# Kernel optimization log

Measured on AMD Instinct MI355X. Metric: run time of the kernel, lower is better.

Reference implementation:

```python
import jax, jax.numpy as jnp
import numpy as np

B, S, H = 2, 2048, 2048
N = 16               # num heads
NOPE, ROPE, V = 128, 64, 128
QHD = NOPE + ROPE    # 192 per-head q/k dim
QL, KVL = 1536, 512  # q_lora_rank, kv_lora_rank
THETA = 10000.0
SCALE = QHD ** -0.5
EPS = 1e-6


def rmsnorm(x, w):
    var = jnp.mean(x.astype(jnp.float32) ** 2, axis=-1, keepdims=True)
    return (x.astype(jnp.float32) * jax.lax.rsqrt(var + EPS)).astype(x.dtype) * w


def rotate_half(x):
    d = x.shape[-1] // 2
    return jnp.concatenate([-x[..., d:], x[..., :d]], axis=-1)


def setup_inputs() -> dict:
    key = jax.random.key(0)
    ks = jax.random.split(key, 8)
    w = lambda k, shape: jax.random.normal(k, shape, jnp.float32) * 0.02
    return {
        "hidden_states": jax.random.normal(ks[0], (B, S, H), jnp.float32),
        "position_ids": (jnp.arange(B * S, dtype=jnp.int64) % 4096).reshape(B, S),
        "q_a_w": w(ks[1], (QL, H)),
        "q_a_ln_w": jnp.ones((QL,), jnp.float32),
        "q_b_w": w(ks[2], (N * QHD, QL)),
        "kv_a_w": w(ks[3], (KVL + ROPE, H)),
        "kv_a_ln_w": jnp.ones((KVL,), jnp.float32),
        "kv_b_w": w(ks[4], (N * (NOPE + V), KVL)),
        "o_w": w(ks[5], (H, N * V)),
    }


def mla_forward(hidden_states, position_ids, q_a_w, q_a_ln_w, q_b_w,
                kv_a_w, kv_a_ln_w, kv_b_w, o_w):
    b, s, _ = hidden_states.shape
    # ---- Q low-rank path: q_b(rmsnorm(q_a(x))) ----
    q = rmsnorm(hidden_states @ q_a_w.T, q_a_ln_w) @ q_b_w.T
    q = q.reshape(b, s, N, QHD)
    q_nope, q_pe = q[..., :NOPE], q[..., NOPE:]
    # ---- compressed KV + shared rope key ----
    kv_a = hidden_states @ kv_a_w.T                       # [b,s,KVL+ROPE]
    compressed_kv = rmsnorm(kv_a[..., :KVL], kv_a_ln_w)   # [b,s,KVL]
    k_pe = kv_a[..., KVL:].reshape(b, s, 1, ROPE)         # MQA rope key
    # ---- RoPE (default, theta=1e4) from position_ids ----
    inv_freq = 1.0 / (THETA ** (jnp.arange(0, ROPE, 2, dtype=jnp.float32) / ROPE))
    freqs = position_ids.astype(jnp.float32)[..., None] * inv_freq  # [b,s,ROPE/2]
    emb = jnp.concatenate([freqs, freqs], axis=-1)                  # [b,s,ROPE]
    cos = jnp.cos(emb)[:, :, None, :].astype(hidden_states.dtype)   # [b,s,1,ROPE]
    sin = jnp.sin(emb)[:, :, None, :].astype(hidden_states.dtype)
    q_pe = q_pe * cos + rotate_half(q_pe) * sin
    k_pe = k_pe * cos + rotate_half(k_pe) * sin
    # ---- decompress latent KV via kv_b_proj ----
    kv = (compressed_kv @ kv_b_w.T).reshape(b, s, N, NOPE + V)
    k_nope, v = kv[..., :NOPE], kv[..., NOPE:]
    k = jnp.concatenate([k_nope, jnp.broadcast_to(k_pe, (b, s, N, ROPE))], axis=-1)
    qf = jnp.concatenate([q_nope, q_pe], axis=-1)          # [b,s,N,QHD]
    # ---- causal SDPA in bsnd layout ----
    scores = jnp.einsum('bqnd,bknd->bnqk', qf, k) * SCALE  # [b,N,s,s]
    causal = jnp.tril(jnp.ones((s, s), bool))
    scores = jnp.where(causal, scores, jnp.finfo(scores.dtype).min)
    probs = jax.nn.softmax(scores, axis=-1)
    attn = jnp.einsum('bnqk,bknd->bqnd', probs, v)         # [b,s,N,V]
    out = attn.reshape(b, s, N * V) @ o_w.T
    return out


def reference(hidden_states, position_ids, q_a_w, q_a_ln_w, q_b_w,
              kv_a_w, kv_a_ln_w, kv_b_w, o_w):
    return mla_forward(hidden_states, position_ids, q_a_w, q_a_ln_w, q_b_w,
                       kv_a_w, kv_a_ln_w, kv_b_w, o_w)
```

## Files before the change

kernel.cpp:

```cpp
#include <hip/hip_runtime.h>
#include <cstdio>

typedef unsigned short u16;
typedef u16 u16x8 __attribute__((ext_vector_type(8)));
typedef __bf16 bf16x8 __attribute__((ext_vector_type(8)));
typedef float f32x4 __attribute__((ext_vector_type(4)));

#define AS1 __attribute__((address_space(1)))
#define AS3 __attribute__((address_space(3)))

#define GLOAD16(gsrc, ldst) __builtin_amdgcn_global_load_lds( \
    (const AS1 void*)(gsrc), (AS3 void*)(ldst), 16, 0, 0)

__device__ __forceinline__ u16 f2bf(float f) {
  unsigned u = __builtin_bit_cast(unsigned, f);
  u += 0x7fffu + ((u >> 16) & 1u);
  return (u16)(u >> 16);
}
__device__ __forceinline__ float bf2f(u16 h) {
  return __builtin_bit_cast(float, (unsigned)h << 16);
}

__global__ __launch_bounds__(256) void cvt_pad_k(const float* __restrict__ src,
                                                 u16* __restrict__ dst,
                                                 long srcN, long dstN) {
  long i = ((long)blockIdx.x * 256 + threadIdx.x) * 8;
  const long stride = (long)gridDim.x * 256 * 8;
  for (; i < dstN; i += stride) {
    u16x8 o = {0,0,0,0,0,0,0,0};
    if (i < srcN) {
      const float4* p = (const float4*)(src + i);
      float4 a = p[0], b = p[1];
      o[0]=f2bf(a.x); o[1]=f2bf(a.y); o[2]=f2bf(a.z); o[3]=f2bf(a.w);
      o[4]=f2bf(b.x); o[5]=f2bf(b.y); o[6]=f2bf(b.z); o[7]=f2bf(b.w);
    }
    *(u16x8*)(dst + i) = o;
  }
}

__global__ __launch_bounds__(256) void rms_k(const u16* __restrict__ src, u16* __restrict__ dst,
                                             const float* __restrict__ w,
                                             int sstride, int dstride, int cols) {
  const int row = blockIdx.x;
  const int tid = threadIdx.x;
  const int nch = cols >> 3;
  float x[8];
  float ss = 0.f;
  if (tid < nch) {
    u16x8 v = *(const u16x8*)(src + (size_t)row * sstride + tid * 8);
#pragma unroll
    for (int j = 0; j < 8; ++j) { x[j] = bf2f(v[j]); ss += x[j] * x[j]; }
  } else {
#pragma unroll
    for (int j = 0; j < 8; ++j) x[j] = 0.f;
  }
#pragma unroll
  for (int off = 1; off < 64; off <<= 1) ss += __shfl_xor(ss, off);
  __shared__ float red[4];
  const int wv = tid >> 6, ln = tid & 63;
  if (ln == 0) red[wv] = ss;
  __syncthreads();
  const float tot = red[0] + red[1] + red[2] + red[3];
  const float rs = 1.0f / sqrtf(tot / (float)cols + 1e-6f);
  if (tid < nch) {
    u16x8 o;
#pragma unroll
    for (int j = 0; j < 8; ++j) o[j] = f2bf(x[j] * rs * w[tid * 8 + j]);
    *(u16x8*)(dst + (size_t)row * dstride + tid * 8) = o;
  }
}

__global__ __launch_bounds__(256) void rope_k(u16* __restrict__ q, const u16* __restrict__ kva,
                                              u16* __restrict__ kpe, const int* __restrict__ pos) {
  const int tok = blockIdx.x;
  const int j = threadIdx.x & 63;
  const int w = threadIdx.x >> 6;
  const float p = (float)pos[tok];
  const int jj = j & 31;
  const float inv = __powf(10000.0f, -(float)jj * (1.0f / 32.0f));
  float s, c;
  __sincosf(p * inv, &s, &c);
  const float sgn = (j < 32) ? -1.0f : 1.0f;
  const int partner = (j < 32) ? j + 32 : j - 32;
  if (w == 0) {
    const float x  = bf2f(kva[(size_t)tok * 640 + 512 + j]);
    const float xp = bf2f(kva[(size_t)tok * 640 + 512 + partner]);
    kpe[(size_t)tok * 64 + j] = f2bf(x * c + sgn * xp * s);
  }
#pragma unroll
  for (int hh = 0; hh < 4; ++hh) {
    const int h = w * 4 + hh;
    const size_t base = (size_t)tok * 3072 + h * 192 + 128;
    const float x  = bf2f(q[base + j]);
    const float xp = bf2f(q[base + partner]);
    q[base + j] = f2bf(x * c + sgn * xp * s);
  }
}

__global__ __launch_bounds__(256) void gemm_bt(const u16* __restrict__ A, const u16* __restrict__ B,
                                               u16* __restrict__ Cb, float* __restrict__ Cf,
                                               int M, int N, int K) {
  __shared__ __attribute__((aligned(16))) u16 As[128 * 64];
  __shared__ __attribute__((aligned(16))) u16 Bs[128 * 64];
  const int tid = threadIdx.x;
  const int m0 = blockIdx.y * 128, n0 = blockIdx.x * 128;
  const int w = tid >> 6, lane = tid & 63;
  const int wr = w >> 1, wc = w & 1;
  const int lr = lane & 15, g = lane >> 4;

  f32x4 acc[4][4] = {};

  for (int k0 = 0; k0 < K; k0 += 64) {
#pragma unroll
    for (int i = 0; i < 4; ++i) {
      const int c = i * 256 + tid;
      const int row = c >> 3, col = (c & 7) << 3;
      GLOAD16(A + (size_t)(m0 + row) * K + k0 + col, &As[c * 8]);
    }
#pragma unroll
    for (int i = 0; i < 4; ++i) {
      const int c = i * 256 + tid;
      const int row = c >> 3, col = (c & 7) << 3;
      GLOAD16(B + (size_t)(n0 + row) * K + k0 + col, &Bs[c * 8]);
    }
    __syncthreads();
    bf16x8 af[4][2], bfr[4][2];
#pragma unroll
    for (int x = 0; x < 4; ++x)
#pragma unroll
      for (int kk = 0; kk < 2; ++kk) {
        af[x][kk]  = *(const bf16x8*)(&As[(wr * 64 + x * 16 + lr) * 64 + kk * 32 + g * 8]);
        bfr[x][kk] = *(const bf16x8*)(&Bs[(wc * 64 + x * 16 + lr) * 64 + kk * 32 + g * 8]);
      }
#pragma unroll
    for (int mi = 0; mi < 4; ++mi)
#pragma unroll
      for (int ni = 0; ni < 4; ++ni)
#pragma unroll
        for (int kk = 0; kk < 2; ++kk)
          acc[mi][ni] = __builtin_amdgcn_mfma_f32_16x16x32_bf16(af[mi][kk], bfr[ni][kk],
                                                                acc[mi][ni], 0, 0, 0);
    __syncthreads();
  }

  const int rb = m0 + wr * 64, cb = n0 + wc * 64;
#pragma unroll
  for (int mi = 0; mi < 4; ++mi)
#pragma unroll
    for (int ni = 0; ni < 4; ++ni)
#pragma unroll
      for (int i = 0; i < 4; ++i) {
        const int r = rb + mi * 16 + g * 4 + i;
        const int cI = cb + ni * 16 + lr;
        if (Cf) Cf[(size_t)r * N + cI] = acc[mi][ni][i];
        else    Cb[(size_t)r * N + cI] = f2bf(acc[mi][ni][i]);
      }
}

__global__ __launch_bounds__(512) void gemm256(const u16* __restrict__ A, const u16* __restrict__ B,
                                               u16* __restrict__ Cb, float* __restrict__ Cf,
                                               int M, int N, int K) {
  __shared__ __attribute__((aligned(16))) u16 As[2][256 * 64];
  __shared__ __attribute__((aligned(16))) u16 Bs[2][256 * 64];
  const int tid = threadIdx.x;
  const int m0 = blockIdx.y * 256, n0 = blockIdx.x * 256;
  const int wid = tid >> 6, lane = tid & 63;
  const int wr = wid >> 2, wc = wid & 3;
  const int lr = lane & 15, g = lane >> 4;

  const u16* pA[4];
  const u16* pB[4];
  int lOff[4];
#pragma unroll
  for (int i = 0; i < 4; ++i) {
    const int c = i * 512 + tid;
    const int row = c >> 3, cl = c & 7;
    const int cg = cl ^ (row & 7);
    lOff[i] = c * 8;
    pA[i] = A + (size_t)(m0 + row) * K + cg * 8;
    pB[i] = B + (size_t)(n0 + row) * K + cg * 8;
  }

  const int aBase = (wr * 128 + lr) * 64;
  const int bBase = (wc * 64 + lr) * 64;
  int kch[2];
#pragma unroll
  for (int kk = 0; kk < 2; ++kk) kch[kk] = ((kk * 4 + g) ^ (lr & 7)) * 8;

  f32x4 acc[8][4] = {};
  const int nkt = K >> 6;

#pragma unroll
  for (int i = 0; i < 4; ++i) GLOAD16(pA[i], &As[0][lOff[i]]);
#pragma unroll
  for (int i = 0; i < 4; ++i) GLOAD16(pB[i], &Bs[0][lOff[i]]);
#pragma unroll
  for (int i = 0; i < 4; ++i) { pA[i] += 64; pB[i] += 64; }
  asm volatile("s_waitcnt vmcnt(0)" ::: "memory");
  __builtin_amdgcn_s_barrier();
  __builtin_amdgcn_sched_barrier(0);

  for (int t = 0; t < nkt; ++t) {
    const int buf = t & 1;
    if (t + 1 < nkt) {
#pragma unroll
      for (int i = 0; i < 4; ++i) GLOAD16(pA[i], &As[buf ^ 1][lOff[i]]);
#pragma unroll
      for (int i = 0; i < 4; ++i) GLOAD16(pB[i], &Bs[buf ^ 1][lOff[i]]);
#pragma unroll
      for (int i = 0; i < 4; ++i) { pA[i] += 64; pB[i] += 64; }
    }
    bf16x8 bfr[4][2];
#pragma unroll
    for (int fn = 0; fn < 4; ++fn)
#pragma unroll
      for (int kk = 0; kk < 2; ++kk)
        bfr[fn][kk] = *(const bf16x8*)(&Bs[buf][bBase + fn * 1024 + kch[kk]]);
#pragma unroll
    for (int q = 0; q < 4; ++q) {
      bf16x8 afr[2][2];
#pragma unroll
      for (int fr = 0; fr < 2; ++fr)
#pragma unroll
        for (int kk = 0; kk < 2; ++kk)
          afr[fr][kk] = *(const bf16x8*)(&As[buf][aBase + (q * 2 + fr) * 1024 + kch[kk]]);
      asm volatile("s_waitcnt lgkmcnt(0)" ::: "memory");
      __builtin_amdgcn_sched_barrier(0);
      __builtin_amdgcn_s_setprio(1);
#pragma unroll
      for (int fr = 0; fr < 2; ++fr)
#pragma unroll
        for (int fn = 0; fn < 4; ++fn)
#pragma unroll
          for (int kk = 0; kk < 2; ++kk)
            acc[q * 2 + fr][fn] = __builtin_amdgcn_mfma_f32_16x16x32_bf16(
                afr[fr][kk], bfr[fn][kk], acc[q * 2 + fr][fn], 0, 0, 0);
      __builtin_amdgcn_s_setprio(0);
      if (q == 3) asm volatile("s_waitcnt vmcnt(0)" ::: "memory");
      __builtin_amdgcn_s_barrier();
    }
    __builtin_amdgcn_sched_barrier(0);
  }

  const int rb = m0 + wr * 128, cb = n0 + wc * 64;
#pragma unroll
  for (int fm = 0; fm < 8; ++fm)
#pragma unroll
    for (int fn = 0; fn < 4; ++fn)
#pragma unroll
      for (int i = 0; i < 4; ++i) {
        const int r = rb + fm * 16 + g * 4 + i;
        const int cI = cb + fn * 16 + lr;
        if (Cf) Cf[(size_t)r * N + cI] = acc[fm][fn][i];
        else    Cb[(size_t)r * N + cI] = f2bf(acc[fm][fn][i]);
      }
}

__global__ __launch_bounds__(256) void vtr_k(const u16* __restrict__ kvb, u16* __restrict__ vT) {
  __shared__ u16 tile[128 * 72];
  const int bh = blockIdx.x, b = bh >> 4, h = bh & 15;
  const int s0 = blockIdx.y * 64;
  const int t = threadIdx.x;
  {
    const int s = t >> 2;
    const int vc = (t & 3) * 32;
    const u16* src = kvb + (size_t)(b * 2048 + s0 + s) * 4096 + h * 256 + 128 + vc;
#pragma unroll
    for (int c = 0; c < 4; ++c) {
      u16x8 v = *(const u16x8*)(src + c * 8);
#pragma unroll
      for (int e = 0; e < 8; ++e) tile[(vc + c * 8 + e) * 72 + s] = v[e];
    }
  }
  __syncthreads();
  {
    const int v = t >> 1;
    const int sh = (t & 1) * 32;
    u16* dst = vT + (size_t)(bh * 128 + v) * 2048 + s0 + sh;
    const u16* srow = &tile[v * 72 + sh];
#pragma unroll
    for (int c = 0; c < 4; ++c)
      *(u16x8*)(dst + c * 8) = *(const u16x8*)(srow + c * 8);
  }
}

__global__ __launch_bounds__(256) void attn_k(const u16* __restrict__ q, const u16* __restrict__ kvb,
                                              const u16* __restrict__ kpe, const u16* __restrict__ vT,
                                              u16* __restrict__ ao) {
  __shared__ __attribute__((aligned(16))) u16 Ks[64 * 192];
  __shared__ __attribute__((aligned(16))) u16 Vt[128 * 64];

  const float SCALE = 0.07216878364870323f;
  const int bh = blockIdx.x;
  const int b = bh >> 4, h = bh & 15;
  const int j = 15 - blockIdx.y;
  const int tid = threadIdx.x, w = tid >> 6, lane = tid & 63;
  const int lr = lane & 15, g = lane >> 4;

  const int q0 = j * 128;
  const int qrb = q0 + w * 32;
  u16* Psw = &Ks[w * 2304];

  bf16x8 qf[2][6];
#pragma unroll
  for (int m = 0; m < 2; ++m)
#pragma unroll
    for (int kd = 0; kd < 6; ++kd)
      qf[m][kd] = *(const bf16x8*)(q + (size_t)(b * 2048 + qrb + m * 16 + lr) * 3072 +
                                   h * 192 + kd * 32 + g * 8);

  float mrow[2][4], lrow[2][4];
  f32x4 o[2][8] = {};
#pragma unroll
  for (int m = 0; m < 2; ++m)
#pragma unroll
    for (int i = 0; i < 4; ++i) { mrow[m][i] = -1e30f; lrow[m][i] = 0.f; }

  const int nt = (q0 >> 6) + 2;
  for (int t = 0; t < nt; ++t) {
    const int k0 = t * 64;
#pragma unroll
    for (int i = 0; i < 6; ++i) {
      const int c = i * 256 + tid;
      const int row = c / 24, cl = c - row * 24;
      const int cg = cl ^ (row & 7);
      const u16* src = (cg < 16)
        ? (kvb + (size_t)(b * 2048 + k0 + row) * 4096 + h * 256 + cg * 8)
        : (kpe + (size_t)(b * 2048 + k0 + row) * 64 + (cg - 16) * 8);
      GLOAD16(src, &Ks[c * 8]);
    }
#pragma unroll
    for (int i = 0; i < 4; ++i) {
      const int c = i * 256 + tid;
      const int v = c >> 3, cl = c & 7;
      const int cg = cl ^ (v & 7);
      GLOAD16(vT + (size_t)(bh * 128 + v) * 2048 + k0 + cg * 8, &Vt[c * 8]);
    }
    __syncthreads();

    const bool active = (k0 <= qrb + 31);
    f32x4 sAcc[2][4] = {};
    if (active) {
#pragma unroll
      for (int nf = 0; nf < 4; ++nf) {
        const int rr = nf * 16 + lr;
#pragma unroll
        for (int kd = 0; kd < 6; ++kd) {
          const int ch = (kd * 4 + g) ^ (rr & 7);
          const bf16x8 kf = *(const bf16x8*)(&Ks[rr * 192 + ch * 8]);
#pragma unroll
          for (int m = 0; m < 2; ++m)
            sAcc[m][nf] = __builtin_amdgcn_mfma_f32_16x16x32_bf16(qf[m][kd], kf, sAcc[m][nf], 0, 0, 0);
        }
      }
    }
    __syncthreads();

    if (active) {
#pragma unroll
      for (int m = 0; m < 2; ++m) {
        float sv[4][4];
#pragma unroll
        for (int nf = 0; nf < 4; ++nf)
#pragma unroll
          for (int i = 0; i < 4; ++i) {
            const int qrow = qrb + m * 16 + g * 4 + i;
            const int kcol = k0 + nf * 16 + lr;
            const float vS = sAcc[m][nf][i] * SCALE;
            sv[nf][i] = (kcol > qrow) ? -1e30f : vS;
          }
        float fac[4], mn[4];
#pragma unroll
        for (int i = 0; i < 4; ++i) {
          float rm = fmaxf(fmaxf(sv[0][i], sv[1][i]), fmaxf(sv[2][i], sv[3][i]));
          rm = fmaxf(rm, __shfl_xor(rm, 1));
          rm = fmaxf(rm, __shfl_xor(rm, 2));
          rm = fmaxf(rm, __shfl_xor(rm, 4));
          rm = fmaxf(rm, __shfl_xor(rm, 8));
          mn[i] = fmaxf(mrow[m][i], rm);
          fac[i] = __expf(mrow[m][i] - mn[i]);
          mrow[m][i] = mn[i];
        }
#pragma unroll
        for (int i = 0; i < 4; ++i) {
          float rsum = 0.f;
#pragma unroll
          for (int nf = 0; nf < 4; ++nf) { sv[nf][i] = __expf(sv[nf][i] - mn[i]); rsum += sv[nf][i]; }
          rsum += __shfl_xor(rsum, 1);
          rsum += __shfl_xor(rsum, 2);
          rsum += __shfl_xor(rsum, 4);
          rsum += __shfl_xor(rsum, 8);
          lrow[m][i] = lrow[m][i] * fac[i] + rsum;
        }
#pragma unroll
        for (int nv = 0; nv < 8; ++nv)
#pragma unroll
          for (int i = 0; i < 4; ++i) o[m][nv][i] *= fac[i];
#pragma unroll
        for (int nf = 0; nf < 4; ++nf)
#pragma unroll
          for (int i = 0; i < 4; ++i)
            Psw[(m * 16 + g * 4 + i) * 72 + nf * 16 + lr] = f2bf(sv[nf][i]);
      }
      asm volatile("s_waitcnt lgkmcnt(0)" ::: "memory");

#pragma unroll
      for (int kc = 0; kc < 2; ++kc) {
        bf16x8 vfr[8];
#pragma unroll
        for (int nv = 0; nv < 8; ++nv) {
          const int v = nv * 16 + lr;
          const int cx = (kc * 4 + g) ^ (v & 7);
          vfr[nv] = *(const bf16x8*)(&Vt[v * 64 + cx * 8]);
        }
#pragma unroll
        for (int m = 0; m < 2; ++m) {
          const bf16x8 pf = *(const bf16x8*)(&Psw[(m * 16 + lr) * 72 + kc * 32 + g * 8]);
#pragma unroll
          for (int nv = 0; nv < 8; ++nv)
            o[m][nv] = __builtin_amdgcn_mfma_f32_16x16x32_bf16(pf, vfr[nv], o[m][nv], 0, 0, 0);
        }
      }
    }
    __syncthreads();
  }

#pragma unroll
  for (int m = 0; m < 2; ++m)
#pragma unroll
    for (int i = 0; i < 4; ++i) {
      const float inv = 1.0f / lrow[m][i];
      const size_t tokOff = (size_t)(b * 2048 + qrb + m * 16 + g * 4 + i) * 2048 + h * 128;
#pragma unroll
      for (int nv = 0; nv < 8; ++nv)
        ao[tokOff + nv * 16 + lr] = f2bf(o[m][nv][i] * inv);
    }
}

extern "C" void kernel_launch(void* const* d_in, const int* in_sizes, int n_in,
                              void* d_out, int out_size, void* d_ws, size_t ws_size,
                              hipStream_t stream) {
  const float* hidden  = (const float*)d_in[0];
  const int*   pos     = (const int*)d_in[1];
  const float* q_a_w   = (const float*)d_in[2];
  const float* q_a_ln  = (const float*)d_in[3];
  const float* q_b_w   = (const float*)d_in[4];
  const float* kv_a_w  = (const float*)d_in[5];
  const float* kv_a_ln = (const float*)d_in[6];
  const float* kv_b_w  = (const float*)d_in[7];
  const float* o_w     = (const float*)d_in[8];
  float* out = (float*)d_out;

  char* ws = (char*)d_ws;
  u16* hb  = (u16*)(ws + 0L);
  u16* w1  = (u16*)(ws + 16777216L);
  u16* w2  = (u16*)(ws + 23068672L);
  u16* w3  = (u16*)(ws + 32505856L);
  u16* w4  = (u16*)(ws + 35127296L);
  u16* w5  = (u16*)(ws + 39321600L);
  u16* qa  = (u16*)(ws + 47710208L);
  u16* qb  = (u16*)(ws + 60293120L);
  u16* kva = (u16*)(ws + 85458944L);
  u16* ckv = (u16*)(ws + 90701824L);
  u16* kpe = (u16*)(ws + 94896128L);
  u16* kvb = (u16*)(ws + 95420416L);
  u16* ao  = (u16*)(ws + 128974848L);
  u16* vT  = hb;
  if (ws_size < 145752064UL) { fprintf(stderr, "ws too small: %zu\n", ws_size); return; }

  auto cvt = [&](const float* s, u16* d, long sn, long dn) {
    long blocks = (dn / 8 + 255) / 256; if (blocks > 2048) blocks = 2048;
    cvt_pad_k<<<dim3((unsigned)blocks), dim3(256), 0, stream>>>(s, d, sn, dn);
  };
  cvt(hidden, hb, 4096L * 2048, 4096L * 2048);
  cvt(q_a_w,  w1, 1536L * 2048, 1536L * 2048);
  cvt(q_b_w,  w2, 3072L * 1536, 3072L * 1536);
  cvt(kv_a_w, w3, 576L * 2048,  640L * 2048);
  cvt(kv_b_w, w4, 4096L * 512,  4096L * 512);
  cvt(o_w,    w5, 2048L * 2048, 2048L * 2048);

  gemm_bt<<<dim3(12, 32), 256, 0, stream>>>(hb, w1, qa, nullptr, 4096, 1536, 2048);
  rms_k<<<4096, 256, 0, stream>>>(qa, qa, q_a_ln, 1536, 1536, 1536);
  gemm256<<<dim3(12, 16), 512, 0, stream>>>(qa, w2, qb, nullptr, 4096, 3072, 1536);
  gemm_bt<<<dim3(5, 32), 256, 0, stream>>>(hb, w3, kva, nullptr, 4096, 640, 2048);
  rms_k<<<4096, 256, 0, stream>>>(kva, ckv, kv_a_ln, 640, 512, 512);
  rope_k<<<4096, 256, 0, stream>>>(qb, kva, kpe, pos);
  gemm256<<<dim3(16, 16), 512, 0, stream>>>(ckv, w4, kvb, nullptr, 4096, 4096, 512);
  vtr_k<<<dim3(32, 32), 256, 0, stream>>>(kvb, vT);
  attn_k<<<dim3(32, 16), 256, 0, stream>>>(qb, kvb, kpe, vT, ao);
  gemm256<<<dim3(8, 16), 512, 0, stream>>>(ao, w5, nullptr, out, 4096, 2048, 2048);
}
```

Before: 471.9 us.

## Fold softmax scale into q_b GEMM and add lazy rescale in attention

Applies the attention scale inside the q_b GEMM epilogue, so the attention kernel no longer multiplies every score. The attention softmax now builds the causal mask only on diagonal tiles and rescales the running max and output accumulators only when some row's max grows by more than a threshold, checked wave-wide. It also raises wave priority around the MFMA sections. The trade-offs are slightly different bf16 rounding of scaled q and an extra branch and vote per tile. The lazy-rescale threshold also lets exp values grow beyond 1 in between rescales.

```diff
diff --git a/kernel.cpp b/kernel.cpp
--- a/kernel.cpp
+++ b/kernel.cpp
@@ -99,7 +99,7 @@
 
 __global__ __launch_bounds__(256) void gemm_bt(const u16* __restrict__ A, const u16* __restrict__ B,
                                                u16* __restrict__ Cb, float* __restrict__ Cf,
-                                               int M, int N, int K) {
+                                               int M, int N, int K, float cs) {
   __shared__ __attribute__((aligned(16))) u16 As[128 * 64];
   __shared__ __attribute__((aligned(16))) u16 Bs[128 * 64];
   const int tid = threadIdx.x;
@@ -152,14 +152,14 @@
       for (int i = 0; i < 4; ++i) {
         const int r = rb + mi * 16 + g * 4 + i;
         const int cI = cb + ni * 16 + lr;
-        if (Cf) Cf[(size_t)r * N + cI] = acc[mi][ni][i];
-        else    Cb[(size_t)r * N + cI] = f2bf(acc[mi][ni][i]);
+        if (Cf) Cf[(size_t)r * N + cI] = acc[mi][ni][i] * cs;
+        else    Cb[(size_t)r * N + cI] = f2bf(acc[mi][ni][i] * cs);
       }
 }
 
 __global__ __launch_bounds__(512) void gemm256(const u16* __restrict__ A, const u16* __restrict__ B,
                                                u16* __restrict__ Cb, float* __restrict__ Cf,
-                                               int M, int N, int K) {
+                                               int M, int N, int K, float cs) {
   __shared__ __attribute__((aligned(16))) u16 As[2][256 * 64];
   __shared__ __attribute__((aligned(16))) u16 Bs[2][256 * 64];
   const int tid = threadIdx.x;
@@ -251,8 +251,8 @@
       for (int i = 0; i < 4; ++i) {
         const int r = rb + fm * 16 + g * 4 + i;
         const int cI = cb + fn * 16 + lr;
-        if (Cf) Cf[(size_t)r * N + cI] = acc[fm][fn][i];
-        else    Cb[(size_t)r * N + cI] = f2bf(acc[fm][fn][i]);
+        if (Cf) Cf[(size_t)r * N + cI] = acc[fm][fn][i] * cs;
+        else    Cb[(size_t)r * N + cI] = f2bf(acc[fm][fn][i] * cs);
       }
 }
 
@@ -290,7 +290,6 @@
   __shared__ __attribute__((aligned(16))) u16 Ks[64 * 192];
   __shared__ __attribute__((aligned(16))) u16 Vt[128 * 64];
 
-  const float SCALE = 0.07216878364870323f;
   const int bh = blockIdx.x;
   const int b = bh >> 4, h = bh & 15;
   const int j = 15 - blockIdx.y;
@@ -341,6 +340,7 @@
     const bool active = (k0 <= qrb + 31);
     f32x4 sAcc[2][4] = {};
     if (active) {
+      __builtin_amdgcn_s_setprio(1);
 #pragma unroll
       for (int nf = 0; nf < 4; ++nf) {
         const int rr = nf * 16 + lr;
@@ -353,23 +353,32 @@
             sAcc[m][nf] = __builtin_amdgcn_mfma_f32_16x16x32_bf16(qf[m][kd], kf, sAcc[m][nf], 0, 0, 0);
         }
       }
+      __builtin_amdgcn_s_setprio(0);
     }
     __syncthreads();
 
     if (active) {
+      const bool needMask = (k0 + 63 > qrb);
 #pragma unroll
       for (int m = 0; m < 2; ++m) {
         float sv[4][4];
-#pragma unroll
-        for (int nf = 0; nf < 4; ++nf)
-#pragma unroll
-          for (int i = 0; i < 4; ++i) {
-            const int qrow = qrb + m * 16 + g * 4 + i;
-            const int kcol = k0 + nf * 16 + lr;
-            const float vS = sAcc[m][nf][i] * SCALE;
-            sv[nf][i] = (kcol > qrow) ? -1e30f : vS;
-          }
-        float fac[4], mn[4];
+        if (needMask) {
+#pragma unroll
+          for (int nf = 0; nf < 4; ++nf)
+#pragma unroll
+            for (int i = 0; i < 4; ++i) {
+              const int qrow = qrb + m * 16 + g * 4 + i;
+              const int kcol = k0 + nf * 16 + lr;
+              sv[nf][i] = (kcol > qrow) ? -1e30f : sAcc[m][nf][i];
+            }
+        } else {
+#pragma unroll
+          for (int nf = 0; nf < 4; ++nf)
+#pragma unroll
+            for (int i = 0; i < 4; ++i) sv[nf][i] = sAcc[m][nf][i];
+        }
+        float rm4[4];
+        bool exceed = false;
 #pragma unroll
         for (int i = 0; i < 4; ++i) {
           float rm = fmaxf(fmaxf(sv[0][i], sv[1][i]), fmaxf(sv[2][i], sv[3][i]));
@@ -377,25 +386,31 @@
           rm = fmaxf(rm, __shfl_xor(rm, 2));
           rm = fmaxf(rm, __shfl_xor(rm, 4));
           rm = fmaxf(rm, __shfl_xor(rm, 8));
-          mn[i] = fmaxf(mrow[m][i], rm);
-          fac[i] = __expf(mrow[m][i] - mn[i]);
-          mrow[m][i] = mn[i];
+          rm4[i] = rm;
+          exceed = exceed || (rm > mrow[m][i] + 8.0f);
+        }
+        if (__any(exceed)) {
+#pragma unroll
+          for (int i = 0; i < 4; ++i) {
+            const float mn = fmaxf(mrow[m][i], rm4[i]);
+            const float fac = __expf(mrow[m][i] - mn);
+            mrow[m][i] = mn;
+            lrow[m][i] *= fac;
+#pragma unroll
+            for (int nv = 0; nv < 8; ++nv) o[m][nv][i] *= fac;
+          }
         }
 #pragma unroll
         for (int i = 0; i < 4; ++i) {
           float rsum = 0.f;
 #pragma unroll
-          for (int nf = 0; nf < 4; ++nf) { sv[nf][i] = __expf(sv[nf][i] - mn[i]); rsum += sv[nf][i]; }
+          for (int nf = 0; nf < 4; ++nf) { sv[nf][i] = __expf(sv[nf][i] - mrow[m][i]); rsum += sv[nf][i]; }
           rsum += __shfl_xor(rsum, 1);
           rsum += __shfl_xor(rsum, 2);
           rsum += __shfl_xor(rsum, 4);
           rsum += __shfl_xor(rsum, 8);
-          lrow[m][i] = lrow[m][i] * fac[i] + rsum;
-        }
-#pragma unroll
-        for (int nv = 0; nv < 8; ++nv)
-#pragma unroll
-          for (int i = 0; i < 4; ++i) o[m][nv][i] *= fac[i];
+          lrow[m][i] += rsum;
+        }
 #pragma unroll
         for (int nf = 0; nf < 4; ++nf)
 #pragma unroll
@@ -404,6 +419,7 @@
       }
       asm volatile("s_waitcnt lgkmcnt(0)" ::: "memory");
 
+      __builtin_amdgcn_s_setprio(1);
 #pragma unroll
       for (int kc = 0; kc < 2; ++kc) {
         bf16x8 vfr[8];
@@ -421,6 +437,7 @@
             o[m][nv] = __builtin_amdgcn_mfma_f32_16x16x32_bf16(pf, vfr[nv], o[m][nv], 0, 0, 0);
         }
       }
+      __builtin_amdgcn_s_setprio(0);
     }
     __syncthreads();
   }
@@ -468,6 +485,8 @@
   u16* vT  = hb;
   if (ws_size < 145752064UL) { fprintf(stderr, "ws too small: %zu\n", ws_size); return; }
 
+  const float SCALE = 0.07216878364870323f;
+
   auto cvt = [&](const float* s, u16* d, long sn, long dn) {
     long blocks = (dn / 8 + 255) / 256; if (blocks > 2048) blocks = 2048;
     cvt_pad_k<<<dim3((unsigned)blocks), dim3(256), 0, stream>>>(s, d, sn, dn);
@@ -479,14 +498,14 @@
   cvt(kv_b_w, w4, 4096L * 512,  4096L * 512);
   cvt(o_w,    w5, 2048L * 2048, 2048L * 2048);
 
-  gemm_bt<<<dim3(12, 32), 256, 0, stream>>>(hb, w1, qa, nullptr, 4096, 1536, 2048);
+  gemm_bt<<<dim3(12, 32), 256, 0, stream>>>(hb, w1, qa, nullptr, 4096, 1536, 2048, 1.0f);
   rms_k<<<4096, 256, 0, stream>>>(qa, qa, q_a_ln, 1536, 1536, 1536);
-  gemm256<<<dim3(12, 16), 512, 0, stream>>>(qa, w2, qb, nullptr, 4096, 3072, 1536);
-  gemm_bt<<<dim3(5, 32), 256, 0, stream>>>(hb, w3, kva, nullptr, 4096, 640, 2048);
+  gemm256<<<dim3(12, 16), 512, 0, stream>>>(qa, w2, qb, nullptr, 4096, 3072, 1536, SCALE);
+  gemm_bt<<<dim3(5, 32), 256, 0, stream>>>(hb, w3, kva, nullptr, 4096, 640, 2048, 1.0f);
   rms_k<<<4096, 256, 0, stream>>>(kva, ckv, kv_a_ln, 640, 512, 512);
   rope_k<<<4096, 256, 0, stream>>>(qb, kva, kpe, pos);
-  gemm256<<<dim3(16, 16), 512, 0, stream>>>(ckv, w4, kvb, nullptr, 4096, 4096, 512);
+  gemm256<<<dim3(16, 16), 512, 0, stream>>>(ckv, w4, kvb, nullptr, 4096, 4096, 512, 1.0f);
   vtr_k<<<dim3(32, 32), 256, 0, stream>>>(kvb, vT);
   attn_k<<<dim3(32, 16), 256, 0, stream>>>(qb, kvb, kpe, vT, ao);
-  gemm256<<<dim3(8, 16), 512, 0, stream>>>(ao, w5, nullptr, out, 4096, 2048, 2048);
-}
+  gemm256<<<dim3(8, 16), 512, 0, stream>>>(ao, w5, nullptr, out, 4096, 2048, 2048, 1.0f);
+}
```

Measured after the change: 456.9 us. -3.2%, faster.
